# Kernel optimization log

Measured on AMD Instinct MI355X. Metric: run time of the kernel, lower is better.

The kernel has to match this reference:

```python
import jax, jax.numpy as jnp
import numpy as np

N_NODES = 50000
N_REL = 8
N_EDGES = 64000
D_IN = 128
D_OUT = 128


def setup_inputs() -> dict:
    key = jax.random.key(0)
    k1, k2, k3, k4 = jax.random.split(key, 4)
    features = jax.random.normal(k1, (N_NODES, D_IN), dtype=jnp.float32)
    W = jax.random.normal(k2, (N_REL, D_IN, D_OUT), dtype=jnp.float32) * 0.05
    b = jnp.zeros((N_REL, D_OUT), dtype=jnp.float32)
    src = jax.random.randint(k3, (N_REL, N_EDGES), 0, N_NODES, dtype=jnp.int64)
    dst = jax.random.randint(k4, (N_REL, N_EDGES), 0, N_NODES, dtype=jnp.int64)
    return {"features": features, "W": W, "b": b, "src": src, "dst": dst}


def reference(features, W, b, src, dst):
    # R-GCN layer: per-relation DGL GraphConv (norm='both', bias) summed over relations.
    N = features.shape[0]
    R = W.shape[0]
    out = jnp.zeros((N, W.shape[-1]), dtype=features.dtype)
    for r in range(R):  # fixed small relation count; edges fully vectorized
        s, d = src[r], dst[r]
        ones = jnp.ones(s.shape[0], dtype=features.dtype)
        out_deg = jnp.clip(jax.ops.segment_sum(ones, s, num_segments=N), 1.0)
        in_deg = jnp.clip(jax.ops.segment_sum(ones, d, num_segments=N), 1.0)
        # pre-scale source features by out_degree^-1/2, gather, aggregate to dst
        m = features * (out_deg ** -0.5)[:, None]          # [N, D_in]
        agg = jax.ops.segment_sum(m[s], d, num_segments=N)  # [N, D_in]
        # weight after aggregation (in_feats == out_feats path), then dst norm + bias
        rst = (agg @ W[r]) * (in_deg ** -0.5)[:, None] + b[r]
        out = out + rst  # HeteroGraphConv aggregate='sum'
    return out
```

## Files before the change

### kernel.cpp

```cpp
#include <hip/hip_runtime.h>

#define N_NODES 50000
#define N_REL 8
#define N_EDGES 64000
#define D 128
#define TROWS 32
#define NT 1563
#define CAP 128
#define SLABW 66

typedef __attribute__((ext_vector_type(8))) short short8;
typedef __attribute__((ext_vector_type(4))) float f32x4;

__device__ __forceinline__ unsigned short f2bf(float x) {
  unsigned int u = __float_as_uint(x);
  u += 0x7FFFu + ((u >> 16) & 1u);
  return (unsigned short)(u >> 16);
}
__device__ __forceinline__ float bflo(unsigned v) { return __uint_as_float(v << 16); }
__device__ __forceinline__ float bfhi(unsigned v) { return __uint_as_float(v & 0xFFFF0000u); }
__device__ __forceinline__ unsigned packbf(float x, float y) {
  return (unsigned)f2bf(x) | ((unsigned)f2bf(y) << 16);
}

__global__ __launch_bounds__(256) void setup_kernel(
    const int* __restrict__ src, const int* __restrict__ dst,
    const float* __restrict__ F, const float* __restrict__ W,
    const float* __restrict__ b, int* __restrict__ outc, int* __restrict__ inc,
    uint2* __restrict__ F16, unsigned short* __restrict__ Wt,
    float* __restrict__ bs) {
  int bid = blockIdx.x, t = threadIdx.x;
  if (bid < 2000) {
    int i = bid * 256 + t;
    int r = i / N_EDGES;
    atomicAdd(&outc[r * N_NODES + src[i]], 1);
    atomicAdd(&inc[r * N_NODES + dst[i]], 1);
  } else if (bid < 8250) {
    int i = (bid - 2000) * 256 + t;
    float4 v = ((const float4*)F)[i];
    uint2 o;
    o.x = packbf(v.x, v.y);
    o.y = packbf(v.z, v.w);
    F16[i] = o;
  } else {
    int i = (bid - 8250) * 256 + t;
    int r = i >> 14, rem = i & 16383, n = rem >> 7, k = rem & 127;
    Wt[i] = f2bf(W[(r << 14) + (k << 7) + n]);
    if (bid == 8250 && t < D) {
      float v = 0.f;
#pragma unroll
      for (int rr = 0; rr < N_REL; ++rr) v += b[rr * D + t];
      bs[t] = v;
    }
  }
}

__global__ __launch_bounds__(256) void bucket_kernel(
    const int* __restrict__ src, const int* __restrict__ dst,
    const int* __restrict__ outc, const int* __restrict__ inc,
    int* __restrict__ bcnt, int2* __restrict__ buckets) {
  int i = blockIdx.x * 256 + threadIdx.x;
  int r = i / N_EDGES;
  int s = src[i], d = dst[i];
  float c = rsqrtf(fmaxf((float)outc[r * N_NODES + s], 1.0f)) *
            rsqrtf(fmaxf((float)inc[r * N_NODES + d], 1.0f));
  int tile = d >> 5;
  int slot = atomicAdd(&bcnt[r * NT + tile], 1);
  if (slot < CAP)
    buckets[(size_t)(r * NT + tile) * CAP + slot] =
        make_int2(s | ((d & 31) << 17), __float_as_int(c));
}

__global__ __launch_bounds__(512, 2) void fused_kernel(
    const unsigned int* __restrict__ F16,
    const unsigned short* __restrict__ Wt,
    const int* __restrict__ bcnt,
    const int2* __restrict__ buckets,
    const float* __restrict__ bs,
    float* __restrict__ out) {
  __shared__ unsigned slabs[8][TROWS * SLABW];
  __shared__ int2 dlds[8][CAP];
  int tid = threadIdx.x;
  int lane = tid & 63;
  int w = __builtin_amdgcn_readfirstlane(tid >> 6);
  int l15 = lane & 15, g = lane >> 4;

  short8 bfr[8][4];
#pragma unroll
  for (int r = 0; r < 8; ++r)
#pragma unroll
    for (int ks = 0; ks < 4; ++ks)
      bfr[r][ks] = *(const short8*)&Wt[(size_t)r * D * D +
                                       (w * 16 + l15) * D + ks * 32 + g * 8];
  float bias = bs[w * 16 + l15];

#define RMW(dd, fv)                                           \
  {                                                           \
    int row_ = ((dd).x >> 17) & 31;                           \
    unsigned* p_ = &slabs[w][row_ * SLABW + lane];            \
    float c_ = __int_as_float((dd).y);                        \
    unsigned old_ = *p_;                                      \
    float vx_ = fmaf(c_, bflo(fv), bflo(old_));               \
    float vy_ = fmaf(c_, bfhi(fv), bfhi(old_));               \
    *p_ = packbf(vx_, vy_);                                   \
  }

  for (int t = blockIdx.x; t < NT; t += 256) {
    __syncthreads();

    for (int i = lane; i < TROWS * SLABW; i += 64) slabs[w][i] = 0u;

    int n = min(bcnt[w * NT + t], CAP);
    const int2* bk = &buckets[(size_t)(w * NT + t) * CAP];
    if (lane < n) dlds[w][lane] = bk[lane];
    if (lane + 64 < n) dlds[w][lane + 64] = bk[lane + 64];

    int i = 0;
    for (; i + 4 <= n; i += 4) {
      int2 d0 = dlds[w][i], d1 = dlds[w][i + 1], d2 = dlds[w][i + 2],
           d3 = dlds[w][i + 3];
      unsigned f0 = F16[(unsigned)(d0.x & 0x1FFFF) * 64 + lane];
      unsigned f1 = F16[(unsigned)(d1.x & 0x1FFFF) * 64 + lane];
      unsigned f2 = F16[(unsigned)(d2.x & 0x1FFFF) * 64 + lane];
      unsigned f3 = F16[(unsigned)(d3.x & 0x1FFFF) * 64 + lane];
      RMW(d0, f0) RMW(d1, f1) RMW(d2, f2) RMW(d3, f3)
    }
    for (; i < n; ++i) {
      int2 dd = dlds[w][i];
      unsigned fv = F16[(unsigned)(dd.x & 0x1FFFF) * 64 + lane];
      RMW(dd, fv)
    }

    __syncthreads();

    f32x4 a0 = (f32x4){0.f, 0.f, 0.f, 0.f};
    f32x4 a1 = (f32x4){0.f, 0.f, 0.f, 0.f};
#pragma unroll
    for (int r = 0; r < 8; ++r) {
#pragma unroll
      for (int ks = 0; ks < 4; ++ks) {
        short8 A0 = *(const short8*)&slabs[r][l15 * SLABW + ks * 16 + g * 4];
        short8 A1 =
            *(const short8*)&slabs[r][(16 + l15) * SLABW + ks * 16 + g * 4];
        a0 = __builtin_amdgcn_mfma_f32_16x16x32_bf16(A0, bfr[r][ks], a0, 0, 0, 0);
        a1 = __builtin_amdgcn_mfma_f32_16x16x32_bf16(A1, bfr[r][ks], a1, 0, 0, 0);
      }
    }

    int t0 = t * TROWS;
    int col = w * 16 + l15;
#pragma unroll
    for (int q = 0; q < 4; ++q) {
      int row0 = t0 + g * 4 + q;
      if (row0 < N_NODES) out[(size_t)row0 * D + col] = a0[q] + bias;
      int row1 = t0 + 16 + g * 4 + q;
      if (row1 < N_NODES) out[(size_t)row1 * D + col] = a1[q] + bias;
    }
  }
#undef RMW
}

extern "C" void kernel_launch(void* const* d_in, const int* in_sizes, int n_in,
                              void* d_out, int out_size, void* d_ws, size_t ws_size,
                              hipStream_t stream) {
  const float* F = (const float*)d_in[0];
  const float* W = (const float*)d_in[1];
  const float* b = (const float*)d_in[2];
  const int* src = (const int*)d_in[3];
  const int* dst = (const int*)d_in[4];
  float* out = (float*)d_out;

  char* ws = (char*)d_ws;
  size_t o = 0;
  int* outc = (int*)(ws + o);  o += (size_t)N_REL * N_NODES * 4;
  int* inc = (int*)(ws + o);   o += (size_t)N_REL * N_NODES * 4;
  int* bcnt = (int*)(ws + o);  o += (size_t)N_REL * NT * 4;
  size_t zero_bytes = o;
  int2* buckets = (int2*)(ws + o);               o += (size_t)N_REL * NT * CAP * 8;
  unsigned int* F16 = (unsigned int*)(ws + o);   o += (size_t)N_NODES * 64 * 4;
  unsigned short* Wt = (unsigned short*)(ws + o); o += (size_t)N_REL * D * D * 2;
  float* bs = (float*)(ws + o);                  o += D * 4;

  hipMemsetAsync(outc, 0, zero_bytes, stream);
  setup_kernel<<<8762, 256, 0, stream>>>(src, dst, F, W, b, outc, inc,
                                         (uint2*)F16, Wt, bs);
  bucket_kernel<<<2000, 256, 0, stream>>>(src, dst, outc, inc, bcnt, buckets);
  fused_kernel<<<256, 512, 0, stream>>>(F16, Wt, bcnt, buckets, bs, out);
}
```

Before: 176.8 us.

## Fold edge bucketing into setup and apply per-node degree scales in fused kernel

Edge bucketing moves into the setup kernel, so the separate pass over edges that computed per-edge coefficients is removed. Descriptors shrink to a packed 32-bit word. A small kernel now computes per-node rsqrt degree scales: the out-degree scale is gathered per source in the aggregation loop, and the in-degree scale is applied per destination row before the MFMA. Tiles are halved to 16 rows with a larger grid and a higher occupancy target. The `__launch_bounds__(512, 6)` hint may squeeze registers enough to spill the preloaded weight fragments.

```diff
diff --git a/kernel.cpp b/kernel.cpp
--- a/kernel.cpp
+++ b/kernel.cpp
@@ -4,10 +4,11 @@
 #define N_REL 8
 #define N_EDGES 64000
 #define D 128
-#define TROWS 32
-#define NT 1563
-#define CAP 128
+#define TROWS 16
+#define NT 3125
+#define CAP 64
 #define SLABW 66
+#define GRID 1042
 
 typedef __attribute__((ext_vector_type(8))) short short8;
 typedef __attribute__((ext_vector_type(4))) float f32x4;
@@ -27,14 +28,21 @@
     const int* __restrict__ src, const int* __restrict__ dst,
     const float* __restrict__ F, const float* __restrict__ W,
     const float* __restrict__ b, int* __restrict__ outc, int* __restrict__ inc,
+    int* __restrict__ bcnt, unsigned* __restrict__ bdesc,
     uint2* __restrict__ F16, unsigned short* __restrict__ Wt,
     float* __restrict__ bs) {
   int bid = blockIdx.x, t = threadIdx.x;
   if (bid < 2000) {
     int i = bid * 256 + t;
     int r = i / N_EDGES;
-    atomicAdd(&outc[r * N_NODES + src[i]], 1);
-    atomicAdd(&inc[r * N_NODES + dst[i]], 1);
+    int s = src[i], d = dst[i];
+    atomicAdd(&outc[r * N_NODES + s], 1);
+    atomicAdd(&inc[r * N_NODES + d], 1);
+    int tile = d >> 4;
+    int slot = atomicAdd(&bcnt[r * NT + tile], 1);
+    if (slot < CAP)
+      bdesc[(size_t)(r * NT + tile) * CAP + slot] =
+          (unsigned)s | ((unsigned)(d & 15) << 17);
   } else if (bid < 8250) {
     int i = (bid - 2000) * 256 + t;
     float4 v = ((const float4*)F)[i];
@@ -55,34 +63,25 @@
   }
 }
 
-__global__ __launch_bounds__(256) void bucket_kernel(
-    const int* __restrict__ src, const int* __restrict__ dst,
-    const int* __restrict__ outc, const int* __restrict__ inc,
-    int* __restrict__ bcnt, int2* __restrict__ buckets) {
+__global__ __launch_bounds__(256) void scales_kernel(
+    const int* __restrict__ cnt, float* __restrict__ sc) {
   int i = blockIdx.x * 256 + threadIdx.x;
-  int r = i / N_EDGES;
-  int s = src[i], d = dst[i];
-  float c = rsqrtf(fmaxf((float)outc[r * N_NODES + s], 1.0f)) *
-            rsqrtf(fmaxf((float)inc[r * N_NODES + d], 1.0f));
-  int tile = d >> 5;
-  int slot = atomicAdd(&bcnt[r * NT + tile], 1);
-  if (slot < CAP)
-    buckets[(size_t)(r * NT + tile) * CAP + slot] =
-        make_int2(s | ((d & 31) << 17), __float_as_int(c));
+  if (i < 2 * N_REL * N_NODES) sc[i] = rsqrtf(fmaxf((float)cnt[i], 1.0f));
 }
 
-__global__ __launch_bounds__(512, 2) void fused_kernel(
+__global__ __launch_bounds__(512, 6) void fused_kernel(
     const unsigned int* __restrict__ F16,
     const unsigned short* __restrict__ Wt,
     const int* __restrict__ bcnt,
-    const int2* __restrict__ buckets,
+    const unsigned* __restrict__ bdesc,
+    const float* __restrict__ oscv,
+    const float* __restrict__ iscv,
     const float* __restrict__ bs,
     float* __restrict__ out) {
   __shared__ unsigned slabs[8][TROWS * SLABW];
-  __shared__ int2 dlds[8][CAP];
-  int tid = threadIdx.x;
-  int lane = tid & 63;
-  int w = __builtin_amdgcn_readfirstlane(tid >> 6);
+  __shared__ unsigned dlds[8][CAP];
+  int lane = threadIdx.x & 63;
+  int w = __builtin_amdgcn_readfirstlane(threadIdx.x >> 6);
   int l15 = lane & 15, g = lane >> 4;
 
   short8 bfr[8][4];
@@ -93,69 +92,71 @@
       bfr[r][ks] = *(const short8*)&Wt[(size_t)r * D * D +
                                        (w * 16 + l15) * D + ks * 32 + g * 8];
   float bias = bs[w * 16 + l15];
+  const float* osc = oscv + w * N_NODES;
+  const float* isc = iscv + w * N_NODES;
 
-#define RMW(dd, fv)                                           \
-  {                                                           \
-    int row_ = ((dd).x >> 17) & 31;                           \
-    unsigned* p_ = &slabs[w][row_ * SLABW + lane];            \
-    float c_ = __int_as_float((dd).y);                        \
-    unsigned old_ = *p_;                                      \
-    float vx_ = fmaf(c_, bflo(fv), bflo(old_));               \
-    float vy_ = fmaf(c_, bfhi(fv), bfhi(old_));               \
-    *p_ = packbf(vx_, vy_);                                   \
+#define RMW(dd, cc, fv)                                        \
+  {                                                            \
+    int row_ = ((dd) >> 17) & 15;                              \
+    unsigned* p_ = &slabs[w][row_ * SLABW + lane];             \
+    unsigned old_ = *p_;                                       \
+    *p_ = packbf(fmaf(cc, bflo(fv), bflo(old_)),               \
+                 fmaf(cc, bfhi(fv), bfhi(old_)));              \
   }
 
-  for (int t = blockIdx.x; t < NT; t += 256) {
+  for (int t = blockIdx.x; t < NT; t += GRID) {
     __syncthreads();
 
     for (int i = lane; i < TROWS * SLABW; i += 64) slabs[w][i] = 0u;
 
     int n = min(bcnt[w * NT + t], CAP);
-    const int2* bk = &buckets[(size_t)(w * NT + t) * CAP];
+    const unsigned* bk = &bdesc[(size_t)(w * NT + t) * CAP];
     if (lane < n) dlds[w][lane] = bk[lane];
-    if (lane + 64 < n) dlds[w][lane + 64] = bk[lane + 64];
 
     int i = 0;
     for (; i + 4 <= n; i += 4) {
-      int2 d0 = dlds[w][i], d1 = dlds[w][i + 1], d2 = dlds[w][i + 2],
-           d3 = dlds[w][i + 3];
-      unsigned f0 = F16[(unsigned)(d0.x & 0x1FFFF) * 64 + lane];
-      unsigned f1 = F16[(unsigned)(d1.x & 0x1FFFF) * 64 + lane];
-      unsigned f2 = F16[(unsigned)(d2.x & 0x1FFFF) * 64 + lane];
-      unsigned f3 = F16[(unsigned)(d3.x & 0x1FFFF) * 64 + lane];
-      RMW(d0, f0) RMW(d1, f1) RMW(d2, f2) RMW(d3, f3)
+      unsigned d0 = dlds[w][i], d1 = dlds[w][i + 1], d2 = dlds[w][i + 2],
+               d3 = dlds[w][i + 3];
+      int s0 = d0 & 0x1FFFF, s1 = d1 & 0x1FFFF, s2 = d2 & 0x1FFFF,
+          s3 = d3 & 0x1FFFF;
+      float c0 = osc[s0], c1 = osc[s1], c2 = osc[s2], c3 = osc[s3];
+      unsigned f0 = F16[(unsigned)s0 * 64 + lane];
+      unsigned f1 = F16[(unsigned)s1 * 64 + lane];
+      unsigned f2 = F16[(unsigned)s2 * 64 + lane];
+      unsigned f3 = F16[(unsigned)s3 * 64 + lane];
+      RMW(d0, c0, f0) RMW(d1, c1, f1) RMW(d2, c2, f2) RMW(d3, c3, f3)
     }
     for (; i < n; ++i) {
-      int2 dd = dlds[w][i];
-      unsigned fv = F16[(unsigned)(dd.x & 0x1FFFF) * 64 + lane];
-      RMW(dd, fv)
+      unsigned dd = dlds[w][i];
+      int s0 = dd & 0x1FFFF;
+      float c0 = osc[s0];
+      unsigned fv = F16[(unsigned)s0 * 64 + lane];
+      RMW(dd, c0, fv)
+    }
+
+    int t0 = t * TROWS;
+#pragma unroll
+    for (int ii = 0; ii < TROWS; ++ii) {
+      float c = isc[t0 + ii];
+      unsigned v = slabs[w][ii * SLABW + lane];
+      slabs[w][ii * SLABW + lane] = packbf(bflo(v) * c, bfhi(v) * c);
     }
 
     __syncthreads();
 
-    f32x4 a0 = (f32x4){0.f, 0.f, 0.f, 0.f};
-    f32x4 a1 = (f32x4){0.f, 0.f, 0.f, 0.f};
+    f32x4 acc = (f32x4){0.f, 0.f, 0.f, 0.f};
 #pragma unroll
-    for (int r = 0; r < 8; ++r) {
+    for (int r = 0; r < 8; ++r)
 #pragma unroll
       for (int ks = 0; ks < 4; ++ks) {
-        short8 A0 = *(const short8*)&slabs[r][l15 * SLABW + ks * 16 + g * 4];
-        short8 A1 =
-            *(const short8*)&slabs[r][(16 + l15) * SLABW + ks * 16 + g * 4];
-        a0 = __builtin_amdgcn_mfma_f32_16x16x32_bf16(A0, bfr[r][ks], a0, 0, 0, 0);
-        a1 = __builtin_amdgcn_mfma_f32_16x16x32_bf16(A1, bfr[r][ks], a1, 0, 0, 0);
+        short8 A = *(const short8*)&slabs[r][l15 * SLABW + ks * 16 + g * 4];
+        acc = __builtin_amdgcn_mfma_f32_16x16x32_bf16(A, bfr[r][ks], acc, 0, 0, 0);
       }
-    }
 
-    int t0 = t * TROWS;
     int col = w * 16 + l15;
 #pragma unroll
-    for (int q = 0; q < 4; ++q) {
-      int row0 = t0 + g * 4 + q;
-      if (row0 < N_NODES) out[(size_t)row0 * D + col] = a0[q] + bias;
-      int row1 = t0 + 16 + g * 4 + q;
-      if (row1 < N_NODES) out[(size_t)row1 * D + col] = a1[q] + bias;
-    }
+    for (int q = 0; q < 4; ++q)
+      out[(size_t)(t0 + g * 4 + q) * D + col] = acc[q] + bias;
   }
 #undef RMW
 }
@@ -176,14 +177,16 @@
   int* inc = (int*)(ws + o);   o += (size_t)N_REL * N_NODES * 4;
   int* bcnt = (int*)(ws + o);  o += (size_t)N_REL * NT * 4;
   size_t zero_bytes = o;
-  int2* buckets = (int2*)(ws + o);               o += (size_t)N_REL * NT * CAP * 8;
-  unsigned int* F16 = (unsigned int*)(ws + o);   o += (size_t)N_NODES * 64 * 4;
+  float* oscv = (float*)(ws + o);  o += (size_t)N_REL * N_NODES * 4;
+  float* iscv = (float*)(ws + o);  o += (size_t)N_REL * N_NODES * 4;
+  unsigned* bdesc = (unsigned*)(ws + o);          o += (size_t)N_REL * NT * CAP * 4;
+  unsigned int* F16 = (unsigned int*)(ws + o);    o += (size_t)N_NODES * 64 * 4;
   unsigned short* Wt = (unsigned short*)(ws + o); o += (size_t)N_REL * D * D * 2;
-  float* bs = (float*)(ws + o);                  o += D * 4;
+  float* bs = (float*)(ws + o);                   o += D * 4;
 
   hipMemsetAsync(outc, 0, zero_bytes, stream);
-  setup_kernel<<<8762, 256, 0, stream>>>(src, dst, F, W, b, outc, inc,
-                                         (uint2*)F16, Wt, bs);
-  bucket_kernel<<<2000, 256, 0, stream>>>(src, dst, outc, inc, bcnt, buckets);
-  fused_kernel<<<256, 512, 0, stream>>>(F16, Wt, bcnt, buckets, bs, out);
+  setup_kernel<<<8762, 256, 0, stream>>>(src, dst, F, W, b, outc, inc, bcnt,
+                                         bdesc, (uint2*)F16, Wt, bs);
+  scales_kernel<<<(2 * N_REL * N_NODES + 255) / 256, 256, 0, stream>>>(outc, oscv);
+  fused_kernel<<<GRID, 512, 0, stream>>>(F16, Wt, bcnt, bdesc, oscv, iscv, bs, out);
 }
```

After: 235.5 us. +33.2%, slower.
